# Kernel optimization log

Hardware: AMD Instinct MI355X
Metric: run time of the kernel (lower is better)

The kernel has to match this reference:

```python
import jax, jax.numpy as jnp
import numpy as np

DIM = 512
H = 48
W = 48
WS = 6
NH = 16
HEAD = DIM // NH
SCALE = HEAD ** -0.5
MLP_RATIO = 4
EPS = 1e-3  # keras LayerNormalization default epsilon
B = 16
L = H * W
M = WS * WS
NW = (H // WS) * (W // WS)


def _rel_pos_index(ws):
    # replicates tf.meshgrid (indexing='xy') construction exactly
    ch = np.arange(ws)
    cw = np.arange(ws)
    coords = np.stack(np.meshgrid(ch, cw))              # (2, ws, ws)
    cf = coords.reshape(2, -1)                          # (2, M)
    cf1 = np.concatenate([cf, np.zeros((2, 1), cf.dtype)], axis=1)  # (2, M+1) with global (0,0)
    rel = cf[:, :, None] - cf1[:, None, :]              # (2, M, M+1)
    rel = rel.transpose(1, 2, 0).copy()
    rel[:, :, 0] += ws - 1
    rel[:, :, 1] += ws - 1
    rel[:, :, 0] *= 2 * ws - 1
    return rel.sum(-1)                                  # (M, M+1)

REL_IDX = jnp.asarray(_rel_pos_index(WS))


def layernorm(x, g, b):
    m = x.mean(-1, keepdims=True)
    v = ((x - m) ** 2).mean(-1, keepdims=True)
    return (x - m) / jnp.sqrt(v + EPS) * g + b


def setup_inputs() -> dict:
    key = jax.random.key(0)
    ks = jax.random.split(key, 8)
    dense = lambda k, i, o: jax.random.normal(k, (i, o), jnp.float32) * (1.0 / np.sqrt(i))
    return dict(
        x=jax.random.normal(ks[0], (B, L, DIM), jnp.float32),
        xavg=jax.random.normal(ks[1], (B, 1, DIM), jnp.float32),
        w_kv=dense(ks[2], DIM, 2 * DIM), b_kv=jnp.zeros((2 * DIM,), jnp.float32),
        w_q=dense(ks[3], DIM, DIM), b_q=jnp.zeros((DIM,), jnp.float32),
        rel_bias_table=jax.random.normal(ks[4], ((2 * WS - 1) ** 2, NH), jnp.float32) * 0.02,
        g1=jnp.ones((DIM,), jnp.float32), be1=jnp.zeros((DIM,), jnp.float32),
        g2=jnp.ones((DIM,), jnp.float32), be2=jnp.zeros((DIM,), jnp.float32),
        w_fc1=dense(ks[5], DIM, MLP_RATIO * DIM), b_fc1=jnp.zeros((MLP_RATIO * DIM,), jnp.float32),
        w_fc2=dense(ks[6], MLP_RATIO * DIM, DIM), b_fc2=jnp.zeros((DIM,), jnp.float32),
    )


def _heads(t):
    # (B*, N, C) -> (B*, NH, N, HEAD)
    return t.reshape(t.shape[0], t.shape[1], NH, HEAD).transpose(0, 2, 1, 3)


def _forward(x, xavg, w_kv, b_kv, w_q, b_q, rel_bias_table, g1, be1, g2, be2,
             w_fc1, b_fc1, w_fc2, b_fc2):
    shortcut, shortcut_avg = x, xavg
    xn = layernorm(x, g1, be1)                          # (B, L, C)
    xavgn = layernorm(xavg, g1, be1)                    # (B, 1, C)

    # window partition: (B, L, C) -> (B*NW, M, C)
    xw = xn.reshape(B, H // WS, WS, W // WS, WS, DIM)
    xw = xw.transpose(0, 1, 3, 2, 4, 5).reshape(B * NW, M, DIM)

    # per-window tokens + repeated global token as keys/values
    xavgR = jnp.repeat(xavgn, NW, axis=0)               # (B*NW, 1, C), batch-major like tf.repeat
    x_c = jnp.concatenate([xw, xavgR], axis=1)          # (B*NW, M+1, C)

    kv = x_c @ w_kv + b_kv                              # (B*NW, M+1, 2C)
    q = xw @ w_q + b_q                                  # (B*NW, M, C)
    q_avg = xavgn @ w_q + b_q                           # (B, 1, C)
    kv_g = xn @ w_kv + b_kv                             # (B, L, 2C)

    k, v = jnp.split(kv, 2, axis=-1)
    kg, vg = jnp.split(kv_g, 2, axis=-1)

    qh = _heads(q) * SCALE                              # (B*NW, NH, M, HEAD)
    attn = jnp.einsum('bhqd,bhkd->bhqk', qh, _heads(k))  # (B*NW, NH, M, M+1)
    bias = rel_bias_table[REL_IDX.reshape(-1)].reshape(M, M + 1, NH)
    attn = attn + bias.transpose(2, 0, 1)[None]
    attn = jax.nn.softmax(attn, axis=-1)
    xo = jnp.einsum('bhqk,bhkd->bhqd', attn, _heads(v))
    xo = xo.transpose(0, 2, 1, 3).reshape(B * NW, M, DIM)

    # global token attends to all tokens
    qg = _heads(q_avg) * SCALE                          # (B, NH, 1, HEAD)
    attng = jax.nn.softmax(jnp.einsum('bhqd,bhkd->bhqk', qg, _heads(kg)), axis=-1)
    xavg_o = jnp.einsum('bhqk,bhkd->bhqd', attng, _heads(vg))
    xavg_o = xavg_o.transpose(0, 2, 1, 3).reshape(B, 1, DIM)

    # window reverse: (B*NW, M, C) -> (B, L, C)
    xr = xo.reshape(B, H // WS, W // WS, WS, WS, DIM)
    xr = xr.transpose(0, 1, 3, 2, 4, 5).reshape(B, L, DIM)

    x = shortcut + xr
    xavg = shortcut_avg + xavg_o

    mlp = lambda t: jax.nn.gelu(t @ w_fc1 + b_fc1, approximate=False) @ w_fc2 + b_fc2
    x = x + mlp(layernorm(x, g2, be2))
    xavg = xavg + mlp(layernorm(xavg, g2, be2))
    return x, xavg


def reference(x, xavg, w_kv, b_kv, w_q, b_q, rel_bias_table, g1, be1, g2, be2,
              w_fc1, b_fc1, w_fc2, b_fc2):
    return _forward(x, xavg, w_kv, b_kv, w_q, b_q, rel_bias_table, g1, be1, g2, be2,
                    w_fc1, b_fc1, w_fc2, b_fc2)
```

## Files before the change

### kernel.cpp

```cpp
#include <hip/hip_runtime.h>
#include <stdint.h>

#define DIM 512
#define NHEAD 16
#define HEADD 32
#define BATCH 16
#define SEQL 2304
#define XROWS (BATCH*SEQL)
#define NROWS (XROWS + BATCH)
#define ATT_SCALE 0.17677669529663687f

typedef __attribute__((ext_vector_type(8))) short short8;
typedef __attribute__((ext_vector_type(4))) float f32x4;

__device__ __forceinline__ float bf2f(unsigned short v) {
    union { unsigned u; float f; } t; t.u = ((unsigned)v) << 16; return t.f;
}
__device__ __forceinline__ unsigned short f2bf(float f) {
    union { float f; unsigned u; } t; t.f = f;
    unsigned r = t.u + 0x7fffu + ((t.u >> 16) & 1u);
    return (unsigned short)(r >> 16);
}
__device__ __forceinline__ void unpack8(const int4 c, float* o) {
    union { unsigned u; float f; } t;
    unsigned w0 = (unsigned)c.x, w1 = (unsigned)c.y, w2 = (unsigned)c.z, w3 = (unsigned)c.w;
    t.u = w0 << 16;         o[0] = t.f;
    t.u = w0 & 0xffff0000u; o[1] = t.f;
    t.u = w1 << 16;         o[2] = t.f;
    t.u = w1 & 0xffff0000u; o[3] = t.f;
    t.u = w2 << 16;         o[4] = t.f;
    t.u = w2 & 0xffff0000u; o[5] = t.f;
    t.u = w3 << 16;         o[6] = t.f;
    t.u = w3 & 0xffff0000u; o[7] = t.f;
}
__device__ __forceinline__ void gl_lds16(const void* g, void* l) {
    __builtin_amdgcn_global_load_lds((const __attribute__((address_space(1))) unsigned int*)g,
                                     (__attribute__((address_space(3))) unsigned int*)l,
                                     16, 0, 0);
}

__global__ __launch_bounds__(256) void tpose_kernel(const float* __restrict__ w_q,
                                                    const float* __restrict__ w_kv,
                                                    const float* __restrict__ w_fc1,
                                                    const float* __restrict__ w_fc2,
                                                    unsigned short* __restrict__ Wqkv_t,
                                                    unsigned short* __restrict__ Wfc1_t,
                                                    unsigned short* __restrict__ Wfc2_t) {
    __shared__ float tile[32][33];
    int t = blockIdx.x;
    const float* src; unsigned short* dst;
    int Kd, Nd, rowOff, tk;
    if (t < 256)        { src = w_q;   dst = Wqkv_t; Kd = 512;  Nd = 512;  rowOff = 0;   tk = 16; }
    else if (t < 768)   { t -= 256;  src = w_kv;  dst = Wqkv_t; Kd = 512;  Nd = 1024; rowOff = 512; tk = 16; }
    else if (t < 1792)  { t -= 768;  src = w_fc1; dst = Wfc1_t; Kd = 512;  Nd = 2048; rowOff = 0;   tk = 16; }
    else                { t -= 1792; src = w_fc2; dst = Wfc2_t; Kd = 2048; Nd = 512;  rowOff = 0;   tk = 64; }
    int k0 = (t % tk) * 32;
    int n0 = (t / tk) * 32;
    int tx = threadIdx.x & 31, ty = threadIdx.x >> 5;
    #pragma unroll
    for (int r = 0; r < 32; r += 8)
        tile[r + ty][tx] = src[(long)(k0 + r + ty) * Nd + n0 + tx];
    __syncthreads();
    #pragma unroll
    for (int r = 0; r < 32; r += 8)
        dst[(long)(rowOff + n0 + r + ty) * Kd + k0 + tx] = f2bf(tile[tx][r + ty]);
}

__global__ void smallpack_kernel(const float* __restrict__ b_q, const float* __restrict__ b_kv,
                                 const float* __restrict__ rel_table,
                                 float* __restrict__ bqkv, float* __restrict__ bias_exp) {
    int i = blockIdx.x * 256 + threadIdx.x;
    if (i < 1536) { bqkv[i] = (i < 512) ? b_q[i] : b_kv[i - 512]; return; }
    i -= 1536;
    if (i < NHEAD*36*37) {
        int h = i / (36*37); int rem = i % (36*37); int qi = rem / 37; int j = rem % 37;
        int c0m = qi % 6, c1m = qi / 6;
        int c0n = (j < 36) ? (j % 6) : 0;
        int c1n = (j < 36) ? (j / 6) : 0;
        int id = (c0m - c0n + 5) * 11 + (c1m - c1n + 5);
        bias_exp[i] = rel_table[id * NHEAD + h];
    }
}

__global__ __launch_bounds__(256) void ln_kernel(const float* __restrict__ p1,
                                                 const float* __restrict__ p2, int split,
                                                 const float* __restrict__ g, const float* __restrict__ be,
                                                 unsigned short* __restrict__ out, int nrows) {
    int wv = threadIdx.x >> 6, lane = threadIdx.x & 63;
    int r = blockIdx.x * 4 + wv;
    if (r >= nrows) return;
    const float* src = (r < split) ? (p1 + (long)r * DIM) : (p2 + (long)(r - split) * DIM);
    int c0 = lane * 8;
    float4 v0 = *(const float4*)(src + c0);
    float4 v1 = *(const float4*)(src + c0 + 4);
    float s = v0.x+v0.y+v0.z+v0.w + v1.x+v1.y+v1.z+v1.w;
    float q = v0.x*v0.x+v0.y*v0.y+v0.z*v0.z+v0.w*v0.w + v1.x*v1.x+v1.y*v1.y+v1.z*v1.z+v1.w*v1.w;
    for (int m = 1; m < 64; m <<= 1) { s += __shfl_xor(s, m); q += __shfl_xor(q, m); }
    float mean = s * (1.0f/512.0f);
    float var  = q * (1.0f/512.0f) - mean*mean;
    float rs = rsqrtf(var + 1e-3f);
    float4 g0 = *(const float4*)(g + c0);
    float4 g1 = *(const float4*)(g + c0 + 4);
    float4 b0 = *(const float4*)(be + c0);
    float4 b1 = *(const float4*)(be + c0 + 4);
    unsigned short o[8];
    o[0] = f2bf((v0.x-mean)*rs*g0.x + b0.x);
    o[1] = f2bf((v0.y-mean)*rs*g0.y + b0.y);
    o[2] = f2bf((v0.z-mean)*rs*g0.z + b0.z);
    o[3] = f2bf((v0.w-mean)*rs*g0.w + b0.w);
    o[4] = f2bf((v1.x-mean)*rs*g1.x + b1.x);
    o[5] = f2bf((v1.y-mean)*rs*g1.y + b1.y);
    o[6] = f2bf((v1.z-mean)*rs*g1.z + b1.z);
    o[7] = f2bf((v1.w-mean)*rs*g1.w + b1.w);
    *(int4*)(out + (long)r * DIM + c0) = *(const int4*)o;
}

template<bool GELU_ACT, bool OUT_BF16, bool HAS_RES>
__global__ __launch_bounds__(256) void gemm_kernel(const short* __restrict__ A,
                                                   const short* __restrict__ Bt,
                                                   const float* __restrict__ bias,
                                                   void* __restrict__ Cout,
                                                   const float* __restrict__ Res,
                                                   int M, int N, int K) {
    __shared__ short lds_a[128 * 32];
    __shared__ short lds_b[128 * 32];
    const int tid = threadIdx.x;
    const int lane = tid & 63;
    const int wv = tid >> 6;
    const int m0 = blockIdx.y * 128;
    const int n0 = blockIdx.x * 128;
    const int wm = (wv >> 1) * 64;
    const int wn = (wv & 1) * 64;

    f32x4 acc[4][4];
    #pragma unroll
    for (int i = 0; i < 4; i++)
        #pragma unroll
        for (int j = 0; j < 4; j++) { acc[i][j][0]=0.f; acc[i][j][1]=0.f; acc[i][j][2]=0.f; acc[i][j][3]=0.f; }

    const int srow = tid >> 2;
    const int sk = (tid & 3) * 8;
    const short* Aa = A + (long)(m0 + srow) * K + sk;
    const short* Bb = Bt + (long)(n0 + srow) * K + sk;
    short* la = lds_a + tid * 8;
    short* lb = lds_b + tid * 8;

    const int quad = lane >> 4;
    const int l15 = lane & 15;
    const short* ra = lds_a + (wm + l15) * 32 + quad * 8;
    const short* rb = lds_b + (wn + l15) * 32 + quad * 8;

    for (int k0 = 0; k0 < K; k0 += 32) {
        __syncthreads();
        gl_lds16(Aa + k0, la);
        gl_lds16(Aa + (long)64 * K + k0, la + 64 * 32);
        gl_lds16(Bb + k0, lb);
        gl_lds16(Bb + (long)64 * K + k0, lb + 64 * 32);
        __syncthreads();
        short8 af[4], bf[4];
        #pragma unroll
        for (int mt = 0; mt < 4; mt++) af[mt] = *(const short8*)(ra + mt * 16 * 32);
        #pragma unroll
        for (int nt = 0; nt < 4; nt++) bf[nt] = *(const short8*)(rb + nt * 16 * 32);
        #pragma unroll
        for (int mt = 0; mt < 4; mt++)
            #pragma unroll
            for (int nt = 0; nt < 4; nt++)
                acc[mt][nt] = __builtin_amdgcn_mfma_f32_16x16x32_bf16(af[mt], bf[nt], acc[mt][nt], 0, 0, 0);
    }

    #pragma unroll
    for (int mt = 0; mt < 4; mt++) {
        int rbase = m0 + wm + mt * 16 + quad * 4;
        #pragma unroll
        for (int nt = 0; nt < 4; nt++) {
            int col = n0 + wn + nt * 16 + l15;
            float bv = bias[col];
            #pragma unroll
            for (int r = 0; r < 4; r++) {
                int row = rbase + r;
                if (row < M) {
                    float v = acc[mt][nt][r] + bv;
                    if (GELU_ACT) v = 0.5f * v * (1.0f + erff(v * 0.70710678118654752f));
                    if (HAS_RES) v += Res[(long)row * N + col];
                    if (OUT_BF16) ((unsigned short*)Cout)[(long)row * N + col] = f2bf(v);
                    else          ((float*)Cout)[(long)row * N + col] = v;
                }
            }
        }
    }
}

__global__ __launch_bounds__(256) void winattn_kernel(const short* __restrict__ qkv,
                                                      const float* __restrict__ bias_exp,
                                                      const float* __restrict__ xin,
                                                      float* __restrict__ XALL) {
    __shared__ float kvs[4][37 * 64];
    const int tid = threadIdx.x;
    const int wv = tid >> 6;
    const int lane = tid & 63;
    const int gw = blockIdx.x * 4 + wv;
    const int win = gw >> 4;
    const int h = gw & 15;
    const int b = win >> 6;
    const int i1 = (win >> 3) & 7;
    const int i3 = win & 7;

    float* lws = kvs[wv];

    for (int c = lane; c < 296; c += 64) {
        int cc = c;
        int voff = 512;
        int doff = 0;
        if (cc >= 148) { cc -= 148; voff = 1024; doff = 32; }
        int row = cc >> 2;
        int part = cc & 3;
        int grow;
        if (row < 36) { int i2 = row / 6, i4 = row % 6; grow = b * SEQL + (i1*6 + i2) * 48 + i3*6 + i4; }
        else grow = XROWS + b;
        int4 raw = *(const int4*)(qkv + (long)grow * 1536 + voff + h * 32 + part * 8);
        float tmp[8];
        unpack8(raw, tmp);
        float* dstp = &lws[row * 64 + doff + part * 8];
        *(float4*)dstp       = make_float4(tmp[0], tmp[1], tmp[2], tmp[3]);
        *(float4*)(dstp + 4) = make_float4(tmp[4], tmp[5], tmp[6], tmp[7]);
    }
    __syncthreads();

    const int qi = lane;
    if (qi >= 36) return;
    int i2 = qi / 6, i4 = qi % 6;
    const int growq = b * SEQL + (i1*6 + i2) * 48 + i3*6 + i4;

    float qr[32];
    {
        const int4* qp = (const int4*)(qkv + (long)growq * 1536 + h * 32);
        unpack8(qp[0], qr); unpack8(qp[1], qr + 8); unpack8(qp[2], qr + 16); unpack8(qp[3], qr + 24);
        #pragma unroll
        for (int d = 0; d < 32; d++) qr[d] *= ATT_SCALE;
    }

    const float* brow = bias_exp + h * (36*37) + qi * 37;
    float s[37];
    float mx = -1e30f;
    #pragma unroll
    for (int j = 0; j < 37; j++) {
        float kr[32];
        #pragma unroll
        for (int t4 = 0; t4 < 8; t4++) *(float4*)(kr + t4*4) = *(const float4*)(lws + j * 64 + t4 * 4);
        float d0 = 0.f, d1 = 0.f, d2 = 0.f, d3 = 0.f;
        #pragma unroll
        for (int dd = 0; dd < 8; dd++) {
            d0 += qr[dd]      * kr[dd];
            d1 += qr[8 + dd]  * kr[8 + dd];
            d2 += qr[16 + dd] * kr[16 + dd];
            d3 += qr[24 + dd] * kr[24 + dd];
        }
        float sv = (d0 + d1 + d2 + d3) + brow[j];
        s[j] = sv;
        mx = fmaxf(mx, sv);
    }
    float sum = 0.f;
    #pragma unroll
    for (int j = 0; j < 37; j++) { s[j] = __expf(s[j] - mx); sum += s[j]; }
    float inv_sum = 1.0f / sum;

    float o[32];
    #pragma unroll
    for (int dd = 0; dd < 32; dd++) o[dd] = 0.f;
    #pragma unroll
    for (int j = 0; j < 37; j++) {
        float vr[32];
        #pragma unroll
        for (int t4 = 0; t4 < 8; t4++) *(float4*)(vr + t4*4) = *(const float4*)(lws + j * 64 + 32 + t4 * 4);
        float p = s[j];
        #pragma unroll
        for (int dd = 0; dd < 32; dd++) o[dd] += p * vr[dd];
    }

    const float* xi = xin + (long)growq * DIM + h * 32;
    float* xo = XALL + (long)growq * DIM + h * 32;
    #pragma unroll
    for (int v4 = 0; v4 < 8; v4++) {
        float4 xv = *(const float4*)(xi + v4 * 4);
        float4 ov;
        ov.x = xv.x + o[v4*4 + 0] * inv_sum;
        ov.y = xv.y + o[v4*4 + 1] * inv_sum;
        ov.z = xv.z + o[v4*4 + 2] * inv_sum;
        ov.w = xv.w + o[v4*4 + 3] * inv_sum;
        *(float4*)(xo + v4 * 4) = ov;
    }
}

__global__ __launch_bounds__(256) void gattn_kernel(const short* __restrict__ qkv,
                                                    const float* __restrict__ xavg,
                                                    float* __restrict__ XALL) {
    const int b = blockIdx.x >> 4;
    const int h = blockIdx.x & 15;
    const int tid = threadIdx.x;
    __shared__ float qs[32];
    __shared__ float redm[4], redsum[4];
    __shared__ float wout[4][32];
    if (tid < 32) qs[tid] = bf2f(((const unsigned short*)qkv)[(long)(XROWS + b) * 1536 + h * 32 + tid]);
    __syncthreads();
    float qr[32];
    #pragma unroll
    for (int d = 0; d < 32; d++) qr[d] = qs[d];
    float s[9];
    float mx = -1e30f;
    #pragma unroll
    for (int i = 0; i < 9; i++) {
        int t = tid + i * 256;
        const int4* kp = (const int4*)(qkv + (long)(b * SEQL + t) * 1536 + 512 + h * 32);
        float kr[32];
        unpack8(kp[0], kr); unpack8(kp[1], kr + 8); unpack8(kp[2], kr + 16); unpack8(kp[3], kr + 24);
        float d0 = 0.f, d1 = 0.f, d2 = 0.f, d3 = 0.f;
        #pragma unroll
        for (int dd = 0; dd < 8; dd++) {
            d0 += qr[dd] * kr[dd]; d1 += qr[8+dd] * kr[8+dd];
            d2 += qr[16+dd] * kr[16+dd]; d3 += qr[24+dd] * kr[24+dd];
        }
        s[i] = (d0 + d1 + d2 + d3) * ATT_SCALE;
        mx = fmaxf(mx, s[i]);
    }
    for (int m = 1; m < 64; m <<= 1) mx = fmaxf(mx, __shfl_xor(mx, m));
    if ((tid & 63) == 0) redm[tid >> 6] = mx;
    __syncthreads();
    mx = fmaxf(fmaxf(redm[0], redm[1]), fmaxf(redm[2], redm[3]));
    float sum = 0.f;
    #pragma unroll
    for (int i = 0; i < 9; i++) { s[i] = __expf(s[i] - mx); sum += s[i]; }
    for (int m = 1; m < 64; m <<= 1) sum += __shfl_xor(sum, m);
    if ((tid & 63) == 0) redsum[tid >> 6] = sum;
    __syncthreads();
    sum = redsum[0] + redsum[1] + redsum[2] + redsum[3];
    float o[32];
    #pragma unroll
    for (int d = 0; d < 32; d++) o[d] = 0.f;
    #pragma unroll
    for (int i = 0; i < 9; i++) {
        int t = tid + i * 256;
        const int4* vp = (const int4*)(qkv + (long)(b * SEQL + t) * 1536 + 1024 + h * 32);
        float vr[32];
        unpack8(vp[0], vr); unpack8(vp[1], vr + 8); unpack8(vp[2], vr + 16); unpack8(vp[3], vr + 24);
        float p = s[i];
        #pragma unroll
        for (int d = 0; d < 32; d++) o[d] += p * vr[d];
    }
    for (int m = 1; m < 64; m <<= 1) {
        #pragma unroll
        for (int d = 0; d < 32; d++) o[d] += __shfl_xor(o[d], m);
    }
    if ((tid & 63) == 0) {
        #pragma unroll
        for (int d = 0; d < 32; d++) wout[tid >> 6][d] = o[d];
    }
    __syncthreads();
    if (tid < 32) {
        float t = wout[0][tid] + wout[1][tid] + wout[2][tid] + wout[3][tid];
        XALL[(long)(XROWS + b) * DIM + h * 32 + tid] = xavg[b * DIM + h * 32 + tid] + t / sum;
    }
}

extern "C" void kernel_launch(void* const* d_in, const int* in_sizes, int n_in,
                              void* d_out, int out_size, void* d_ws, size_t ws_size,
                              hipStream_t stream) {
    const float* x      = (const float*)d_in[0];
    const float* xavg   = (const float*)d_in[1];
    const float* w_kv   = (const float*)d_in[2];
    const float* b_kv   = (const float*)d_in[3];
    const float* w_q    = (const float*)d_in[4];
    const float* b_q    = (const float*)d_in[5];
    const float* rel    = (const float*)d_in[6];
    const float* g1     = (const float*)d_in[7];
    const float* be1    = (const float*)d_in[8];
    const float* g2     = (const float*)d_in[9];
    const float* be2    = (const float*)d_in[10];
    const float* w_fc1  = (const float*)d_in[11];
    const float* b_fc1  = (const float*)d_in[12];
    const float* w_fc2  = (const float*)d_in[13];
    const float* b_fc2  = (const float*)d_in[14];

    char* ws = (char*)d_ws;
    size_t off = 0;
    auto alloc = [&](size_t bytes) { void* p = ws + off; off += (bytes + 255) & ~(size_t)255; return p; };
    short* qkv_h          = (short*)alloc((size_t)NROWS * 2048 * 2);
    float* XALL           = (float*)alloc((size_t)NROWS * 512 * 4);
    short* xn             = (short*)alloc((size_t)NROWS * 512 * 2);
    unsigned short* Wqkv_t = (unsigned short*)alloc((size_t)1536 * 512 * 2);
    unsigned short* Wfc1_t = (unsigned short*)alloc((size_t)2048 * 512 * 2);
    unsigned short* Wfc2_t = (unsigned short*)alloc((size_t)512 * 2048 * 2);
    float* bqkv           = (float*)alloc(1536 * 4);
    float* bias_exp       = (float*)alloc((size_t)NHEAD * 36 * 37 * 4);

    tpose_kernel<<<2816, 256, 0, stream>>>(w_q, w_kv, w_fc1, w_fc2,
                                           Wqkv_t, Wfc1_t, Wfc2_t);
    smallpack_kernel<<<(1536 + NHEAD*36*37 + 255) / 256, 256, 0, stream>>>(b_q, b_kv, rel, bqkv, bias_exp);
    ln_kernel<<<(NROWS + 3) / 4, 256, 0, stream>>>(x, xavg, XROWS, g1, be1, (unsigned short*)xn, NROWS);
    gemm_kernel<false, true, false><<<dim3(1536 / 128, (NROWS + 127) / 128), 256, 0, stream>>>(
        xn, (const short*)Wqkv_t, bqkv, qkv_h, nullptr, NROWS, 1536, 512);
    winattn_kernel<<<1024 * 16 / 4, 256, 0, stream>>>(qkv_h, bias_exp, x, XALL);
    gattn_kernel<<<256, 256, 0, stream>>>(qkv_h, xavg, XALL);
    ln_kernel<<<(NROWS + 3) / 4, 256, 0, stream>>>(XALL, XALL + (size_t)XROWS * 512, XROWS, g2, be2,
                                                   (unsigned short*)xn, NROWS);
    gemm_kernel<true, true, false><<<dim3(2048 / 128, (NROWS + 127) / 128), 256, 0, stream>>>(
        xn, (const short*)Wfc1_t, b_fc1, qkv_h, nullptr, NROWS, 2048, 512);
    gemm_kernel<false, false, true><<<dim3(512 / 128, (NROWS + 127) / 128), 256, 0, stream>>>(
        qkv_h, (const short*)Wfc2_t, b_fc2, d_out, XALL, NROWS, 512, 2048);
}
```

Before: 814.1 us.

## Double GEMM K-tile to 64 with XOR-swizzled LDS layout

The GEMM main loop now stages a 128x64 K-slice of A and B per iteration instead of 128x32, which halves the number of barrier pairs per K. The LDS layout is XOR-swizzled on 16-byte chunks by row so the MFMA fragment reads avoid bank conflicts. This doubles LDS use per block, which may lower occupancy.

```diff
diff --git a/kernel.cpp b/kernel.cpp
--- a/kernel.cpp
+++ b/kernel.cpp
@@ -122,8 +122,8 @@
                                                    void* __restrict__ Cout,
                                                    const float* __restrict__ Res,
                                                    int M, int N, int K) {
-    __shared__ short lds_a[128 * 32];
-    __shared__ short lds_b[128 * 32];
+    __shared__ short lds_a[128 * 64];
+    __shared__ short lds_b[128 * 64];
     const int tid = threadIdx.x;
     const int lane = tid & 63;
     const int wv = tid >> 6;
@@ -138,30 +138,43 @@
         #pragma unroll
         for (int j = 0; j < 4; j++) { acc[i][j][0]=0.f; acc[i][j][1]=0.f; acc[i][j][2]=0.f; acc[i][j][3]=0.f; }
 
-    const int srow = tid >> 2;
-    const int sk = (tid & 3) * 8;
-    const short* Aa = A + (long)(m0 + srow) * K + sk;
-    const short* Bb = Bt + (long)(n0 + srow) * K + sk;
+    const int srow = tid >> 3;
+    const int ssl  = tid & 7;
+    const int msl  = ssl ^ (srow & 7);
+    const short* Aa = A + (long)(m0 + srow) * K + msl * 8;
+    const short* Bb = Bt + (long)(n0 + srow) * K + msl * 8;
     short* la = lds_a + tid * 8;
     short* lb = lds_b + tid * 8;
 
     const int quad = lane >> 4;
     const int l15 = lane & 15;
-    const short* ra = lds_a + (wm + l15) * 32 + quad * 8;
-    const short* rb = lds_b + (wn + l15) * 32 + quad * 8;
-
-    for (int k0 = 0; k0 < K; k0 += 32) {
+    const short* ra0 = lds_a + (wm + l15) * 64 + ((quad)     ^ (l15 & 7)) * 8;
+    const short* ra1 = lds_a + (wm + l15) * 64 + ((4 + quad) ^ (l15 & 7)) * 8;
+    const short* rb0 = lds_b + (wn + l15) * 64 + ((quad)     ^ (l15 & 7)) * 8;
+    const short* rb1 = lds_b + (wn + l15) * 64 + ((4 + quad) ^ (l15 & 7)) * 8;
+
+    for (int k0 = 0; k0 < K; k0 += 64) {
         __syncthreads();
-        gl_lds16(Aa + k0, la);
-        gl_lds16(Aa + (long)64 * K + k0, la + 64 * 32);
-        gl_lds16(Bb + k0, lb);
-        gl_lds16(Bb + (long)64 * K + k0, lb + 64 * 32);
+        #pragma unroll
+        for (int i = 0; i < 4; i++) {
+            gl_lds16(Aa + (long)(i * 32) * K + k0, la + i * 256 * 8);
+            gl_lds16(Bb + (long)(i * 32) * K + k0, lb + i * 256 * 8);
+        }
         __syncthreads();
         short8 af[4], bf[4];
         #pragma unroll
-        for (int mt = 0; mt < 4; mt++) af[mt] = *(const short8*)(ra + mt * 16 * 32);
-        #pragma unroll
-        for (int nt = 0; nt < 4; nt++) bf[nt] = *(const short8*)(rb + nt * 16 * 32);
+        for (int mt = 0; mt < 4; mt++) af[mt] = *(const short8*)(ra0 + mt * 16 * 64);
+        #pragma unroll
+        for (int nt = 0; nt < 4; nt++) bf[nt] = *(const short8*)(rb0 + nt * 16 * 64);
+        #pragma unroll
+        for (int mt = 0; mt < 4; mt++)
+            #pragma unroll
+            for (int nt = 0; nt < 4; nt++)
+                acc[mt][nt] = __builtin_amdgcn_mfma_f32_16x16x32_bf16(af[mt], bf[nt], acc[mt][nt], 0, 0, 0);
+        #pragma unroll
+        for (int mt = 0; mt < 4; mt++) af[mt] = *(const short8*)(ra1 + mt * 16 * 64);
+        #pragma unroll
+        for (int nt = 0; nt < 4; nt++) bf[nt] = *(const short8*)(rb1 + nt * 16 * 64);
         #pragma unroll
         for (int mt = 0; mt < 4; mt++)
             #pragma unroll
```

New measurement: 777.9 us. 1.05x faster.
